# Kernel optimization log

Hardware: AMD Instinct MI355X
Metric: run time of the kernel (lower is better)

The kernel has to match this reference:

```python
import jax, jax.numpy as jnp
import numpy as np

IN_DIM = 1024
BS, NCROPS = 32, 1024


def setup_inputs() -> dict:
    key = jax.random.key(0)
    ks = jax.random.split(key, 7)
    s = 1.0 / np.sqrt(IN_DIM)
    return {
        "x": jax.random.normal(ks[0], (BS, NCROPS, IN_DIM), jnp.float32),
        "Wq": jax.random.uniform(ks[1], (IN_DIM,), jnp.float32, -s, s),
        "bq": jax.random.uniform(ks[2], (1,), jnp.float32, -s, s),
        "Wk": jax.random.uniform(ks[3], (IN_DIM,), jnp.float32, -s, s),
        "bk": jax.random.uniform(ks[4], (1,), jnp.float32, -s, s),
        "Wv": jax.random.uniform(ks[5], (IN_DIM, IN_DIM), jnp.float32, -s, s),
        "bv": jax.random.uniform(ks[6], (IN_DIM,), jnp.float32, -s, s),
    }


def reference(x, Wq, bq, Wk, bk, Wv, bv):
    # x: (bs, n, d). 1x1 Conv1d over permuted x == per-position linear maps.
    bs, n, d = x.shape
    q = jnp.einsum("bnd,d->bn", x, Wq) + bq  # (bs, n)   query_conv -> 1 channel
    k = jnp.einsum("bnd,d->bn", x, Wk) + bk  # (bs, n)   key_conv   -> 1 channel
    energy = q[:, :, None] * k[:, None, :]    # (bs, n, n) rank-1 outer product (bmm of (n,1)@(1,n))
    attention = jax.nn.softmax(energy, axis=-1)
    v = jnp.einsum("od,bnd->bon", Wv, x) + bv[None, :, None]  # (bs, d, n) value_conv
    out = jnp.einsum("bdn,bnm->bdm", v, attention)            # (bs, d, n)
    # Faithful to torch .view: raw reshape of (bs, d, n) -> (bs, n, d), NOT a transpose.
    out = out.reshape(bs, n, d)
    return (out, attention)
```

## Files before the change

kernel.cpp:

```cpp
#include <hip/hip_runtime.h>
#include <hip/hip_bf16.h>

#define BS  32
#define N   1024
#define DIM 1024

typedef unsigned short u16;
typedef unsigned int   u32;

typedef __attribute__((ext_vector_type(8))) __bf16 bf16x8;
typedef __attribute__((ext_vector_type(4))) float  f32x4;

__device__ __forceinline__ u16 f2bf(float f) {
    u32 u = __builtin_bit_cast(u32, f);
    u = (u + 0x7FFF + ((u >> 16) & 1)) >> 16;
    return (u16)u;
}

__global__ void convert_qk(const float* __restrict__ x,
                           const float* __restrict__ Wq, const float* __restrict__ bq,
                           const float* __restrict__ Wk, const float* __restrict__ bk,
                           const float* __restrict__ Wv,
                           u16* __restrict__ xb, u16* __restrict__ Wvb,
                           float* __restrict__ qv, float* __restrict__ kv)
{
    int gw   = (blockIdx.x * 256 + threadIdx.x) >> 6;
    int lane = threadIdx.x & 63;
    bool isX = gw < BS * N;
    const float* src = isX ? (x + (size_t)gw * DIM) : (Wv + (size_t)(gw - BS * N) * DIM);
    u16*         dst = isX ? (xb + (size_t)gw * DIM) : (Wvb + (size_t)(gw - BS * N) * DIM);
    float qd = 0.f, kd = 0.f;
    #pragma unroll
    for (int i = 0; i < 4; ++i) {
        int e = i * 256 + lane * 4;
        float4 xv = *(const float4*)&src[e];
        uint2 p;
        p.x = (u32)f2bf(xv.x) | ((u32)f2bf(xv.y) << 16);
        p.y = (u32)f2bf(xv.z) | ((u32)f2bf(xv.w) << 16);
        *(uint2*)&dst[e] = p;
        if (isX) {
            float4 wq = *(const float4*)&Wq[e];
            float4 wk = *(const float4*)&Wk[e];
            qd += xv.x * wq.x + xv.y * wq.y + xv.z * wq.z + xv.w * wq.w;
            kd += xv.x * wk.x + xv.y * wk.y + xv.z * wk.z + xv.w * wk.w;
        }
    }
    if (isX) {
        #pragma unroll
        for (int off = 32; off; off >>= 1) {
            qd += __shfl_xor(qd, off);
            kd += __shfl_xor(kd, off);
        }
        if (lane == 0) { qv[gw] = qd + bq[0]; kv[gw] = kd + bk[0]; }
    }
}

__global__ void qz_writer(const float* __restrict__ qv, const float* __restrict__ kvg,
                          float2* __restrict__ qzg)
{
    int blk = blockIdx.x;
    int b   = blk >> 6;
    int r0  = (blk & 63) * 16;
    __shared__ float ks[1024];
    int tid = threadIdx.x;
    #pragma unroll
    for (int i = 0; i < 4; ++i) ks[i * 256 + tid] = kvg[b * N + i * 256 + tid];
    int row = tid >> 4;
    int c16 = tid & 15;
    float qrow = qv[b * N + r0 + row];
    __syncthreads();
    float z = 0.f;
    #pragma unroll 4
    for (int s = 0; s < 16; ++s) {
        const float4 kk = *(const float4*)&ks[(c16 + s * 16) * 4];
        z += __expf(qrow * kk.x) + __expf(qrow * kk.y)
           + __expf(qrow * kk.z) + __expf(qrow * kk.w);
    }
    z += __shfl_xor(z, 1); z += __shfl_xor(z, 2);
    z += __shfl_xor(z, 4); z += __shfl_xor(z, 8);
    if (c16 == 0) qzg[b * N + r0 + row] = make_float2(qrow, 1.0f / z);
}

__global__ void att_tiles(const float2* __restrict__ qzg, const float* __restrict__ kvg,
                          float* __restrict__ att, u16* __restrict__ attT)
{
    int blk  = blockIdx.x;
    int b    = blk >> 8;
    int rest = blk & 255;
    int r0 = (rest >> 4) * 64;
    int c0 = (rest & 15) * 64;
    int tid = threadIdx.x;
    int tx = tid & 15, ty = tid >> 4;

    float q[4], iz[4];
    #pragma unroll
    for (int i = 0; i < 4; ++i) {
        float2 p = qzg[(size_t)b * N + r0 + tx * 4 + i];
        q[i] = p.x; iz[i] = p.y;
    }
    float kvj[4];
    #pragma unroll
    for (int j = 0; j < 4; ++j) kvj[j] = kvg[(size_t)b * N + c0 + ty * 4 + j];

    float e[4][4];
    #pragma unroll
    for (int i = 0; i < 4; ++i)
        #pragma unroll
        for (int j = 0; j < 4; ++j)
            e[i][j] = __expf(q[i] * kvj[j]) * iz[i];

    float* ab = att + (size_t)b * N * N;
    #pragma unroll
    for (int i = 0; i < 4; ++i) {
        float4 o = make_float4(e[i][0], e[i][1], e[i][2], e[i][3]);
        *(float4*)&ab[(size_t)(r0 + tx * 4 + i) * N + c0 + ty * 4] = o;
    }
    u16* tb = attT + (size_t)b * N * N;
    #pragma unroll
    for (int j = 0; j < 4; ++j) {
        uint2 p;
        p.x = (u32)f2bf(e[0][j]) | ((u32)f2bf(e[1][j]) << 16);
        p.y = (u32)f2bf(e[2][j]) | ((u32)f2bf(e[3][j]) << 16);
        *(uint2*)&tb[(size_t)(c0 + ty * 4 + j) * N + r0 + tx * 4] = p;
    }
}


__device__ __forceinline__ void stage_half8(const u16* __restrict__ Aptr,
                                            const u16* __restrict__ Bptr,
                                            int m0b, int n0b, char* smem,
                                            int h, int w, int lane)
{
    if (h >= 64) return;
    int tile = h >> 2, id = h & 3;
    int db   = tile & 1;
    const u16* G = (id < 2) ? Bptr : Aptr;
    int opb   = (id < 2) ? 65536 : 0;
    int row0  = (id < 2) ? n0b : m0b;
    int halfb = (id & 1) * 16384;
    int kb    = tile * 128;
    int cb    = ((lane & 7) ^ (lane >> 3)) << 4;
    #pragma unroll
    for (int i = 0; i < 2; ++i) {
        int lofs = opb + db * 32768 + halfb + (i * 8 + w) * 1024;
        int r    = (id & 1) * 128 + (i * 8 + w) * 8 + (lane >> 3);
        const char* src = (const char*)G + (size_t)(row0 + r) * 2048 + kb + cb;
        __builtin_amdgcn_global_load_lds(
            (const __attribute__((address_space(1))) u32*)src,
            (__attribute__((address_space(3))) u32*)(smem + lofs), 16, 0, 0);
    }
}

template<bool BF16OUT>
__global__ __launch_bounds__(512, 2) void gemm8p(
    const u16* __restrict__ A, size_t aBatch,
    const u16* __restrict__ B, size_t bBatch,
    void* __restrict__ Cv, size_t cBatch,
    const float* __restrict__ bias)
{
    __shared__ char smem[131072];
    int bid = blockIdx.x;
    int lin = (bid & 7) * 64 + (bid >> 3);
    int b   = lin >> 4;
    int t16 = lin & 15;
    int m0b = (t16 >> 2) * 256, n0b = (t16 & 3) * 256;
    const u16* Aptr = A + aBatch * (size_t)b;
    const u16* Bptr = B + bBatch * (size_t)b;

    int tid  = threadIdx.x;
    int w    = tid >> 6, lane = tid & 63;
    int wm   = w >> 2, wn = w & 3;

    f32x4 acc[8][4] = {};
    bf16x8 aP[2][2], aQ[2][2], bF[4][2];

#define LDA_(dst, fi, ks) dst = *(const bf16x8*)(smem + jdb * 32768 + \
        (wm * 128 + (fi) * 16 + (lane & 15)) * 128 + \
        ((((ks) * 64) + ((lane >> 4) << 4)) ^ ((lane & 7) << 4)))
#define LDB_(dst, ni, ks) dst = *(const bf16x8*)(smem + 65536 + jdb * 32768 + \
        (wn * 64 + (ni) * 16 + (lane & 15)) * 128 + \
        ((((ks) * 64) + ((lane >> 4) << 4)) ^ ((lane & 7) << 4)))
#define MFMA_HALF(FI0, AR) do { \
        __builtin_amdgcn_s_setprio(1); \
        _Pragma("unroll") \
        for (int mi = 0; mi < 2; ++mi) \
            _Pragma("unroll") \
            for (int ni = 0; ni < 4; ++ni) \
                _Pragma("unroll") \
                for (int ks = 0; ks < 2; ++ks) \
                    acc[(FI0) + mi][ni] = __builtin_amdgcn_mfma_f32_16x16x32_bf16( \
                        AR[mi][ks], bF[ni][ks], acc[(FI0) + mi][ni], 0, 0, 0); \
        __builtin_amdgcn_s_setprio(0); \
    } while (0)

    #pragma unroll
    for (int h = 0; h < 7; ++h) stage_half8(Aptr, Bptr, m0b, n0b, smem, h, w, lane);
    asm volatile("s_waitcnt vmcnt(6)" ::: "memory");
    __builtin_amdgcn_s_barrier();
    __builtin_amdgcn_sched_barrier(0);

    #pragma unroll 1
    for (int j = 0; j < 16; ++j) {
        const int jdb = j & 1;
        LDA_(aP[0][0], 0, 0); LDA_(aP[0][1], 0, 1);
        LDA_(aP[1][0], 1, 0); LDA_(aP[1][1], 1, 1);
        LDA_(aQ[0][0], 2, 0); LDA_(aQ[0][1], 2, 1);
        LDA_(aQ[1][0], 3, 0); LDA_(aQ[1][1], 3, 1);
        LDB_(bF[0][0], 0, 0); LDB_(bF[0][1], 0, 1);
        LDB_(bF[1][0], 1, 0); LDB_(bF[1][1], 1, 1);
        LDB_(bF[2][0], 2, 0); LDB_(bF[2][1], 2, 1);
        LDB_(bF[3][0], 3, 0); LDB_(bF[3][1], 3, 1);
        stage_half8(Aptr, Bptr, m0b, n0b, smem, 7 + 4 * j, w, lane);
        __builtin_amdgcn_s_barrier();
        asm volatile("s_waitcnt lgkmcnt(0)" ::: "memory");
        MFMA_HALF(0, aP);
        __builtin_amdgcn_s_barrier();
        LDA_(aP[0][0], 4, 0); LDA_(aP[0][1], 4, 1);
        LDA_(aP[1][0], 5, 0); LDA_(aP[1][1], 5, 1);
        stage_half8(Aptr, Bptr, m0b, n0b, smem, 8 + 4 * j, w, lane);
        __builtin_amdgcn_s_barrier();
        asm volatile("s_waitcnt lgkmcnt(0)" ::: "memory");
        MFMA_HALF(2, aQ);
        __builtin_amdgcn_s_barrier();
        LDA_(aQ[0][0], 6, 0); LDA_(aQ[0][1], 6, 1);
        LDA_(aQ[1][0], 7, 0); LDA_(aQ[1][1], 7, 1);
        stage_half8(Aptr, Bptr, m0b, n0b, smem, 9 + 4 * j, w, lane);
        __builtin_amdgcn_s_barrier();
        asm volatile("s_waitcnt lgkmcnt(0)" ::: "memory");
        MFMA_HALF(4, aP);
        __builtin_amdgcn_s_barrier();
        stage_half8(Aptr, Bptr, m0b, n0b, smem, 10 + 4 * j, w, lane);
        __builtin_amdgcn_s_barrier();
        asm volatile("s_waitcnt lgkmcnt(0)" ::: "memory");
        MFMA_HALF(6, aQ);
        if (j < 14)       asm volatile("s_waitcnt vmcnt(6)" ::: "memory");
        else if (j == 14) asm volatile("s_waitcnt vmcnt(0)" ::: "memory");
        __builtin_amdgcn_s_barrier();
        __builtin_amdgcn_sched_barrier(0);
    }
#undef LDA_
#undef LDB_
#undef MFMA_HALF

    int r4 = (lane >> 4) * 4, cc = lane & 15;
    if constexpr (BF16OUT) {
        u16* Cb = (u16*)Cv + cBatch * (size_t)b;
        #pragma unroll
        for (int fi = 0; fi < 8; ++fi)
            #pragma unroll
            for (int ni = 0; ni < 4; ++ni)
                #pragma unroll
                for (int rg = 0; rg < 4; ++rg) {
                    int row = m0b + wm * 128 + fi * 16 + r4 + rg;
                    int col = n0b + wn * 64 + ni * 16 + cc;
                    Cb[(size_t)row * 1024 + col] = f2bf(acc[fi][ni][rg] + bias[row]);
                }
    } else {
        float* Cb = (float*)Cv + cBatch * (size_t)b;
        #pragma unroll
        for (int fi = 0; fi < 8; ++fi)
            #pragma unroll
            for (int ni = 0; ni < 4; ++ni)
                #pragma unroll
                for (int rg = 0; rg < 4; ++rg) {
                    int row = m0b + wm * 128 + fi * 16 + r4 + rg;
                    int col = n0b + wn * 64 + ni * 16 + cc;
                    Cb[(size_t)row * 1024 + col] = acc[fi][ni][rg];
                }
    }
}

extern "C" void kernel_launch(void* const* d_in, const int* in_sizes, int n_in,
                              void* d_out, int out_size, void* d_ws, size_t ws_size,
                              hipStream_t stream)
{
    const float* x  = (const float*)d_in[0];
    const float* Wq = (const float*)d_in[1];
    const float* bq = (const float*)d_in[2];
    const float* Wk = (const float*)d_in[3];
    const float* bk = (const float*)d_in[4];
    const float* Wv = (const float*)d_in[5];
    const float* bv = (const float*)d_in[6];

    float* out = (float*)d_out;
    float* att = out + (size_t)BS * N * N;

    char* ws = (char*)d_ws;
    u16*  xb   = (u16*)ws;
    u16*  vb   = xb + (size_t)BS * N * DIM;
    u16*  Wvb  = vb + (size_t)BS * N * DIM;
    float* qv  = (float*)(Wvb + (size_t)DIM * DIM);
    float* kv  = qv + BS * N;
    float2* qzg = (float2*)(kv + BS * N);
    u16*  attT = (u16*)(qzg + BS * N);

    convert_qk<<<(BS * N + DIM) / 4, 256, 0, stream>>>(x, Wq, bq, Wk, bk, Wv, xb, Wvb, qv, kv);
    qz_writer<<<BS * 64, 256, 0, stream>>>(qv, kv, qzg);
    gemm8p<true><<<512, 512, 0, stream>>>(Wvb, 0, xb, (size_t)N * DIM, vb, (size_t)N * DIM, bv);
    att_tiles<<<BS * 256, 256, 0, stream>>>(qzg, kv, att, attT);
    gemm8p<false><<<512, 512, 0, stream>>>(vb, (size_t)N * DIM, attT, (size_t)N * N, out, (size_t)N * DIM, nullptr);
}
```

Baseline: 524.6 us.

## Regenerate bf16 attention tiles inside second GEMM instead of materializing transpose

```diff
diff --git a/kernel.cpp b/kernel.cpp
--- a/kernel.cpp
+++ b/kernel.cpp
@@ -82,7 +82,7 @@
 }
 
 __global__ void att_tiles(const float2* __restrict__ qzg, const float* __restrict__ kvg,
-                          float* __restrict__ att, u16* __restrict__ attT)
+                          float* __restrict__ att)
 {
     int blk  = blockIdx.x;
     int b    = blk >> 8;
@@ -102,26 +102,15 @@
     #pragma unroll
     for (int j = 0; j < 4; ++j) kvj[j] = kvg[(size_t)b * N + c0 + ty * 4 + j];
 
-    float e[4][4];
-    #pragma unroll
-    for (int i = 0; i < 4; ++i)
-        #pragma unroll
-        for (int j = 0; j < 4; ++j)
-            e[i][j] = __expf(q[i] * kvj[j]) * iz[i];
-
     float* ab = att + (size_t)b * N * N;
     #pragma unroll
     for (int i = 0; i < 4; ++i) {
-        float4 o = make_float4(e[i][0], e[i][1], e[i][2], e[i][3]);
+        float4 o;
+        o.x = __expf(q[i] * kvj[0]) * iz[i];
+        o.y = __expf(q[i] * kvj[1]) * iz[i];
+        o.z = __expf(q[i] * kvj[2]) * iz[i];
+        o.w = __expf(q[i] * kvj[3]) * iz[i];
         *(float4*)&ab[(size_t)(r0 + tx * 4 + i) * N + c0 + ty * 4] = o;
-    }
-    u16* tb = attT + (size_t)b * N * N;
-    #pragma unroll
-    for (int j = 0; j < 4; ++j) {
-        uint2 p;
-        p.x = (u32)f2bf(e[0][j]) | ((u32)f2bf(e[1][j]) << 16);
-        p.y = (u32)f2bf(e[2][j]) | ((u32)f2bf(e[3][j]) << 16);
-        *(uint2*)&tb[(size_t)(c0 + ty * 4 + j) * N + r0 + tx * 4] = p;
     }
 }
 
@@ -151,11 +140,10 @@
     }
 }
 
-template<bool BF16OUT>
 __global__ __launch_bounds__(512, 2) void gemm8p(
     const u16* __restrict__ A, size_t aBatch,
     const u16* __restrict__ B, size_t bBatch,
-    void* __restrict__ Cv, size_t cBatch,
+    u16* __restrict__ C, size_t cBatch,
     const float* __restrict__ bias)
 {
     __shared__ char smem[131072];
@@ -243,31 +231,180 @@
 #undef MFMA_HALF
 
     int r4 = (lane >> 4) * 4, cc = lane & 15;
-    if constexpr (BF16OUT) {
-        u16* Cb = (u16*)Cv + cBatch * (size_t)b;
+    u16* Cb = C + cBatch * (size_t)b;
+    #pragma unroll
+    for (int fi = 0; fi < 8; ++fi)
         #pragma unroll
-        for (int fi = 0; fi < 8; ++fi)
+        for (int ni = 0; ni < 4; ++ni)
             #pragma unroll
-            for (int ni = 0; ni < 4; ++ni)
-                #pragma unroll
-                for (int rg = 0; rg < 4; ++rg) {
-                    int row = m0b + wm * 128 + fi * 16 + r4 + rg;
-                    int col = n0b + wn * 64 + ni * 16 + cc;
-                    Cb[(size_t)row * 1024 + col] = f2bf(acc[fi][ni][rg] + bias[row]);
-                }
-    } else {
-        float* Cb = (float*)Cv + cBatch * (size_t)b;
+            for (int rg = 0; rg < 4; ++rg) {
+                int row = m0b + wm * 128 + fi * 16 + r4 + rg;
+                int col = n0b + wn * 64 + ni * 16 + cc;
+                Cb[(size_t)row * 1024 + col] = f2bf(acc[fi][ni][rg] + bias[row]);
+            }
+}
+
+
+__device__ __forceinline__ void stageA2(const u16* __restrict__ Ap,
+                                        int m0b, char* smem,
+                                        int T, int hh, int w, int lane)
+{
+    int db = T & 1;
+    int kb = T * 128;
+    int cb = ((lane & 7) ^ (lane >> 3)) << 4;
+    #pragma unroll
+    for (int i = 0; i < 2; ++i) {
+        int lofs = db * 32768 + hh * 16384 + (i * 8 + w) * 1024;
+        int r    = hh * 128 + (i * 8 + w) * 8 + (lane >> 3);
+        const char* src = (const char*)Ap + (size_t)(m0b + r) * 2048 + kb + cb;
+        __builtin_amdgcn_global_load_lds(
+            (const __attribute__((address_space(1))) u32*)src,
+            (__attribute__((address_space(3))) u32*)(smem + lofs), 16, 0, 0);
+    }
+}
+
+__global__ __launch_bounds__(512, 2) void gemm2f(
+    const u16* __restrict__ A,
+    const float2* __restrict__ qzg,
+    const float* __restrict__ kvg,
+    float* __restrict__ C)
+{
+    __shared__ char smem[139264];
+    float2* qzs = (float2*)(smem + 131072);
+
+    int bid = blockIdx.x;
+    int lin = (bid & 7) * 64 + (bid >> 3);
+    int b   = lin >> 4;
+    int t16 = lin & 15;
+    int m0b = (t16 >> 2) * 256, n0b = (t16 & 3) * 256;
+    const u16* Aptr = A + (size_t)b * 1024 * 1024;
+
+    int tid  = threadIdx.x;
+    int w    = tid >> 6, lane = tid & 63;
+    int wm   = w >> 2, wn = w & 3;
+
+    float kvr[4];
+    #pragma unroll
+    for (int h = 0; h < 2; ++h)
         #pragma unroll
-        for (int fi = 0; fi < 8; ++fi)
+        for (int i = 0; i < 2; ++i)
+            kvr[h * 2 + i] = kvg[(size_t)b * N + n0b + h * 128 + (i * 8 + w) * 8 + (lane >> 3)];
+
+    f32x4 acc[8][4] = {};
+    bf16x8 aP[2][2], aQ[2][2], bF[4][2];
+
+#define LDA_(dst, fi, ks) dst = *(const bf16x8*)(smem + jdb * 32768 + \
+        (wm * 128 + (fi) * 16 + (lane & 15)) * 128 + \
+        ((((ks) * 64) + ((lane >> 4) << 4)) ^ ((lane & 7) << 4)))
+#define LDB_(dst, ni, ks) dst = *(const bf16x8*)(smem + 65536 + jdb * 32768 + \
+        (wn * 64 + (ni) * 16 + (lane & 15)) * 128 + \
+        ((((ks) * 64) + ((lane >> 4) << 4)) ^ ((lane & 7) << 4)))
+#define MFMA_HALF(FI0, AR) do { \
+        __builtin_amdgcn_s_setprio(1); \
+        _Pragma("unroll") \
+        for (int mi = 0; mi < 2; ++mi) \
+            _Pragma("unroll") \
+            for (int ni = 0; ni < 4; ++ni) \
+                _Pragma("unroll") \
+                for (int ks = 0; ks < 2; ++ks) \
+                    acc[(FI0) + mi][ni] = __builtin_amdgcn_mfma_f32_16x16x32_bf16( \
+                        AR[mi][ks], bF[ni][ks], acc[(FI0) + mi][ni], 0, 0, 0); \
+        __builtin_amdgcn_s_setprio(0); \
+    } while (0)
+
+#define GEN_HALF(Tn, hh) do { \
+        int kidx = (Tn) * 64 + (((lane & 7) ^ (lane >> 3)) << 3); \
+        float4 g0 = *(const float4*)&qzs[kidx]; \
+        float4 g1 = *(const float4*)&qzs[kidx + 2]; \
+        float4 g2 = *(const float4*)&qzs[kidx + 4]; \
+        float4 g3 = *(const float4*)&qzs[kidx + 6]; \
+        _Pragma("unroll") \
+        for (int i = 0; i < 2; ++i) { \
+            float kk = kvr[(hh) * 2 + i]; \
+            union { u32 u[4]; bf16x8 v; } pk; \
+            pk.u[0] = (u32)f2bf(__expf(g0.x * kk) * g0.y) | ((u32)f2bf(__expf(g0.z * kk) * g0.w) << 16); \
+            pk.u[1] = (u32)f2bf(__expf(g1.x * kk) * g1.y) | ((u32)f2bf(__expf(g1.z * kk) * g1.w) << 16); \
+            pk.u[2] = (u32)f2bf(__expf(g2.x * kk) * g2.y) | ((u32)f2bf(__expf(g2.z * kk) * g2.w) << 16); \
+            pk.u[3] = (u32)f2bf(__expf(g3.x * kk) * g3.y) | ((u32)f2bf(__expf(g3.z * kk) * g3.w) << 16); \
+            *(bf16x8*)(smem + 65536 + ((Tn) & 1) * 32768 + (hh) * 16384 + \
+                       (i * 8 + w) * 1024 + lane * 16) = pk.v; \
+        } \
+    } while (0)
+
+    {
+        const char* qsrc = (const char*)(qzg + (size_t)b * N) + w * 1024 + lane * 16;
+        __builtin_amdgcn_global_load_lds(
+            (const __attribute__((address_space(1))) u32*)qsrc,
+            (__attribute__((address_space(3))) u32*)(smem + 131072 + w * 1024), 16, 0, 0);
+    }
+    stageA2(Aptr, m0b, smem, 0, 0, w, lane);
+    stageA2(Aptr, m0b, smem, 0, 1, w, lane);
+    stageA2(Aptr, m0b, smem, 1, 0, w, lane);
+    asm volatile("s_waitcnt vmcnt(6)" ::: "memory");
+    __builtin_amdgcn_s_barrier();
+    GEN_HALF(0, 0);
+    GEN_HALF(0, 1);
+    asm volatile("s_waitcnt lgkmcnt(0)" ::: "memory");
+    asm volatile("s_waitcnt vmcnt(2)" ::: "memory");
+    __builtin_amdgcn_s_barrier();
+    __builtin_amdgcn_sched_barrier(0);
+
+    #pragma unroll 1
+    for (int j = 0; j < 16; ++j) {
+        const int jdb = j & 1;
+        LDA_(aP[0][0], 0, 0); LDA_(aP[0][1], 0, 1);
+        LDA_(aP[1][0], 1, 0); LDA_(aP[1][1], 1, 1);
+        LDA_(aQ[0][0], 2, 0); LDA_(aQ[0][1], 2, 1);
+        LDA_(aQ[1][0], 3, 0); LDA_(aQ[1][1], 3, 1);
+        LDB_(bF[0][0], 0, 0); LDB_(bF[0][1], 0, 1);
+        LDB_(bF[1][0], 1, 0); LDB_(bF[1][1], 1, 1);
+        LDB_(bF[2][0], 2, 0); LDB_(bF[2][1], 2, 1);
+        LDB_(bF[3][0], 3, 0); LDB_(bF[3][1], 3, 1);
+        if (j < 15) stageA2(Aptr, m0b, smem, j + 1, 1, w, lane);
+        __builtin_amdgcn_s_barrier();
+        asm volatile("s_waitcnt lgkmcnt(0)" ::: "memory");
+        MFMA_HALF(0, aP);
+        __builtin_amdgcn_s_barrier();
+        LDA_(aP[0][0], 4, 0); LDA_(aP[0][1], 4, 1);
+        LDA_(aP[1][0], 5, 0); LDA_(aP[1][1], 5, 1);
+        __builtin_amdgcn_s_barrier();
+        asm volatile("s_waitcnt lgkmcnt(0)" ::: "memory");
+        MFMA_HALF(2, aQ);
+        if (j < 15) GEN_HALF(j + 1, 0);
+        __builtin_amdgcn_s_barrier();
+        LDA_(aQ[0][0], 6, 0); LDA_(aQ[0][1], 6, 1);
+        LDA_(aQ[1][0], 7, 0); LDA_(aQ[1][1], 7, 1);
+        __builtin_amdgcn_s_barrier();
+        asm volatile("s_waitcnt lgkmcnt(0)" ::: "memory");
+        MFMA_HALF(4, aP);
+        if (j < 15) GEN_HALF(j + 1, 1);
+        __builtin_amdgcn_s_barrier();
+        if (j < 14) stageA2(Aptr, m0b, smem, j + 2, 0, w, lane);
+        __builtin_amdgcn_s_barrier();
+        asm volatile("s_waitcnt lgkmcnt(0)" ::: "memory");
+        MFMA_HALF(6, aQ);
+        if (j < 14)       asm volatile("s_waitcnt vmcnt(2)" ::: "memory");
+        else if (j == 14) asm volatile("s_waitcnt vmcnt(0)" ::: "memory");
+        __builtin_amdgcn_s_barrier();
+        __builtin_amdgcn_sched_barrier(0);
+    }
+#undef LDA_
+#undef LDB_
+#undef MFMA_HALF
+#undef GEN_HALF
+
+    int r4 = (lane >> 4) * 4, cc = lane & 15;
+    float* Cb = C + (size_t)b * 1024 * 1024;
+    #pragma unroll
+    for (int fi = 0; fi < 8; ++fi)
+        #pragma unroll
+        for (int ni = 0; ni < 4; ++ni)
             #pragma unroll
-            for (int ni = 0; ni < 4; ++ni)
-                #pragma unroll
-                for (int rg = 0; rg < 4; ++rg) {
-                    int row = m0b + wm * 128 + fi * 16 + r4 + rg;
-                    int col = n0b + wn * 64 + ni * 16 + cc;
-                    Cb[(size_t)row * 1024 + col] = acc[fi][ni][rg];
-                }
-    }
+            for (int rg = 0; rg < 4; ++rg) {
+                int row = m0b + wm * 128 + fi * 16 + r4 + rg;
+                int col = n0b + wn * 64 + ni * 16 + cc;
+                Cb[(size_t)row * 1024 + col] = acc[fi][ni][rg];
+            }
 }
 
 extern "C" void kernel_launch(void* const* d_in, const int* in_sizes, int n_in,
@@ -292,11 +429,10 @@
     float* qv  = (float*)(Wvb + (size_t)DIM * DIM);
     float* kv  = qv + BS * N;
     float2* qzg = (float2*)(kv + BS * N);
-    u16*  attT = (u16*)(qzg + BS * N);
 
     convert_qk<<<(BS * N + DIM) / 4, 256, 0, stream>>>(x, Wq, bq, Wk, bk, Wv, xb, Wvb, qv, kv);
     qz_writer<<<BS * 64, 256, 0, stream>>>(qv, kv, qzg);
-    gemm8p<true><<<512, 512, 0, stream>>>(Wvb, 0, xb, (size_t)N * DIM, vb, (size_t)N * DIM, bv);
-    att_tiles<<<BS * 256, 256, 0, stream>>>(qzg, kv, att, attT);
-    gemm8p<false><<<512, 512, 0, stream>>>(vb, (size_t)N * DIM, attT, (size_t)N * N, out, (size_t)N * DIM, nullptr);
-}
+    gemm8p<<<512, 512, 0, stream>>>(Wvb, 0, xb, (size_t)N * DIM, vb, (size_t)N * DIM, bv);
+    gemm2f<<<512, 512, 0, stream>>>(vb, qzg, kv, out);
+    att_tiles<<<BS * 256, 256, 0, stream>>>(qzg, kv, att);
+}
```

Measured after the change: 537.7 us. 1.03x slower.
